# Kernel tuning notes

Measured on AMD Instinct MI355X. Metric: run time of the kernel, lower is better.

## Reference

```python
import jax, jax.numpy as jnp
import numpy as np

B, S, D, H = 16, 512, 1024, 16
DK = D // H
DFF = 4 * D
EPS = 1e-5
NEG = -1e9


def fake_quant(w):
    # EMA int8 symmetric per-tensor fake quantization of weights (inference view)
    scale = jnp.max(jnp.abs(w)) / 127.0
    wq = jnp.round(w / scale) * scale
    # straight-through estimator form (no-op in fwd)
    return w + jax.lax.stop_gradient(wq - w)


def layer_norm(x, g, b):
    mu = jnp.mean(x, axis=-1, keepdims=True)
    var = jnp.mean(jnp.square(x - mu), axis=-1, keepdims=True)
    return (x - mu) * jax.lax.rsqrt(var + EPS) * g + b


def setup_inputs() -> dict:
    key = jax.random.key(0)
    ks = jax.random.split(key, 16)
    std = 0.02
    inp = {
        'x': jax.random.normal(ks[0], (B, S, D), jnp.float32),
        'mask': jax.random.randint(ks[1], (B, 1, S, S), 0, 2, jnp.int32),
        'wq': jax.random.normal(ks[2], (D, D), jnp.float32) * std,
        'bq': jnp.zeros((D,), jnp.float32),
        'wk': jax.random.normal(ks[3], (D, D), jnp.float32) * std,
        'bk': jnp.zeros((D,), jnp.float32),
        'wv': jax.random.normal(ks[4], (D, D), jnp.float32) * std,
        'bv': jnp.zeros((D,), jnp.float32),
        'wo': jax.random.normal(ks[5], (D, D), jnp.float32) * std,
        'bo': jnp.zeros((D,), jnp.float32),
        'w1': jax.random.normal(ks[6], (D, DFF), jnp.float32) * std,
        'b1': jnp.zeros((DFF,), jnp.float32),
        'w2': jax.random.normal(ks[7], (DFF, D), jnp.float32) * std,
        'b2': jnp.zeros((D,), jnp.float32),
        'ln1_g': jnp.ones((D,), jnp.float32),
        'ln1_b': jnp.zeros((D,), jnp.float32),
        'ln2_g': jnp.ones((D,), jnp.float32),
        'ln2_b': jnp.zeros((D,), jnp.float32),
        'layer': 0,
    }
    return inp


def reference(x, mask, wq, bq, wk, bk, wv, bv, wo, bo, w1, b1, w2, b2,
              ln1_g, ln1_b, ln2_g, ln2_b, layer):
    # --- input sublayer: x + attention(LN(x)) (dropout = identity at eval) ---
    h = layer_norm(x, ln1_g, ln1_b)
    q = (h @ fake_quant(wq) + bq).reshape(B, S, H, DK).transpose(0, 2, 1, 3)
    k = (h @ fake_quant(wk) + bk).reshape(B, S, H, DK).transpose(0, 2, 1, 3)
    v = (h @ fake_quant(wv) + bv).reshape(B, S, H, DK).transpose(0, 2, 1, 3)
    scores = jnp.einsum('bhqd,bhkd->bhqk', q, k) * (1.0 / np.sqrt(DK))
    scores = jnp.where(mask == 0, NEG, scores)
    p = jax.nn.softmax(scores, axis=-1)
    attn = jnp.einsum('bhqk,bhkd->bhqd', p, v)
    attn = attn.transpose(0, 2, 1, 3).reshape(B, S, D)
    x = x + (attn @ wo + bo)
    # --- output sublayer: x + FFN(LN(x)), gelu (exact), middle_drop=False ---
    h2 = layer_norm(x, ln2_g, ln2_b)
    ff = jax.nn.gelu(h2 @ w1 + b1, approximate=False) @ w2 + b2
    return x + ff
```

## Files before the change

kernel.cpp:

```cpp
#include <hip/hip_runtime.h>
#include <hip/hip_bf16.h>
#include <math.h>

#define B_   16
#define S_   512
#define D_   1024
#define H_   16
#define DK_  64
#define DFF_ 4096
#define NROW (B_ * S_)
#define NEG_ (-1.0e9f)
#define SCQ_ 0.18033688011112042f

typedef __attribute__((ext_vector_type(8))) short short8v;
typedef __attribute__((ext_vector_type(4))) float f32x4;

__device__ __forceinline__ void load_lds16(const void* g, void* l) {
    __builtin_amdgcn_global_load_lds(
        reinterpret_cast<const __attribute__((address_space(1))) unsigned int*>(
            reinterpret_cast<uintptr_t>(g)),
        reinterpret_cast<__attribute__((address_space(3))) unsigned int*>(
            reinterpret_cast<uintptr_t>(l)),
        16, 0, 0);
}

__device__ __forceinline__ ushort f2bf_raw(float f) {
    __hip_bfloat16 h = __float2bfloat16(f);
    return *(ushort*)&h;
}

__device__ __forceinline__ float gelu_f(float v) {
    return 0.5f * v * (1.0f + erff(v * 0.70710678118654752f));
}

__global__ void zero_scales_k(unsigned int* p) {
    if (threadIdx.x < 3) p[threadIdx.x] = 0u;
}

__global__ void maxabs_k(const float* __restrict__ w, unsigned int* __restrict__ out, int n) {
    float m = 0.f;
    for (int i = blockIdx.x * blockDim.x + threadIdx.x; i < n; i += gridDim.x * blockDim.x)
        m = fmaxf(m, fabsf(w[i]));
#pragma unroll
    for (int off = 1; off < 64; off <<= 1)
        m = fmaxf(m, __shfl_xor(m, off));
    __shared__ float red[4];
    const int wave = threadIdx.x >> 6;
    if ((threadIdx.x & 63) == 0) red[wave] = m;
    __syncthreads();
    if (threadIdx.x == 0) {
        m = fmaxf(fmaxf(red[0], red[1]), fmaxf(red[2], red[3]));
        atomicMax(out, __float_as_uint(m));
    }
}

__global__ __launch_bounds__(256) void maskpack_k(
    const int* __restrict__ mask, unsigned long long* __restrict__ bits) {
    const int g = blockIdx.x * 4 + (threadIdx.x >> 6);
    const unsigned long long bm = __ballot(mask[(size_t)g * 64 + (threadIdx.x & 63)] != 0);
    if ((threadIdx.x & 63) == 0) bits[g] = bm;
}

__global__ __launch_bounds__(256) void transq_k(
    const float* __restrict__ W, const unsigned int* __restrict__ smax,
    __hip_bfloat16* __restrict__ Wt, int K, int N)
{
    __shared__ float t[32][33];
    const int n0 = blockIdx.x * 32, k0 = blockIdx.y * 32;
    const int tx = threadIdx.x, ty = threadIdx.y;
    float scale = 1.0f;
    if (smax) scale = __uint_as_float(*smax) * (1.0f / 127.0f);
#pragma unroll
    for (int i = 0; i < 4; ++i) {
        float v = W[(size_t)(k0 + ty + 8 * i) * N + n0 + tx];
        if (smax) v = rintf(v / scale) * scale;
        t[ty + 8 * i][tx] = v;
    }
    __syncthreads();
#pragma unroll
    for (int i = 0; i < 4; ++i)
        Wt[(size_t)(n0 + ty + 8 * i) * K + k0 + tx] = __float2bfloat16(t[tx][ty + 8 * i]);
}

__global__ __launch_bounds__(256) void ln_bf16_k(
    const float* __restrict__ x, const float* __restrict__ g,
    const float* __restrict__ b, __hip_bfloat16* __restrict__ y)
{
    const int row = blockIdx.x;
    const int tid = threadIdx.x;
    const float4 v = *(const float4*)&x[(size_t)row * D_ + tid * 4];

    float s = v.x + v.y + v.z + v.w;
#pragma unroll
    for (int off = 1; off < 64; off <<= 1) s += __shfl_xor(s, off);
    __shared__ float red[8];
    const int wave = tid >> 6, lane = tid & 63;
    if (lane == 0) red[wave] = s;
    __syncthreads();
    s = red[0] + red[1] + red[2] + red[3];
    const float mu = s * (1.0f / (float)D_);

    const float d0 = v.x - mu, d1 = v.y - mu, d2 = v.z - mu, d3 = v.w - mu;
    float sq = d0 * d0 + d1 * d1 + d2 * d2 + d3 * d3;
#pragma unroll
    for (int off = 1; off < 64; off <<= 1) sq += __shfl_xor(sq, off);
    if (lane == 0) red[4 + wave] = sq;
    __syncthreads();
    sq = red[4] + red[5] + red[6] + red[7];
    const float rs = 1.0f / sqrtf(sq * (1.0f / (float)D_) + 1e-5f);

    const float4 gv = *(const float4*)&g[tid * 4];
    const float4 bv = *(const float4*)&b[tid * 4];
    union { ushort4 u4; ushort u[4]; } cv;
    cv.u[0] = f2bf_raw(d0 * rs * gv.x + bv.x);
    cv.u[1] = f2bf_raw(d1 * rs * gv.y + bv.y);
    cv.u[2] = f2bf_raw(d2 * rs * gv.z + bv.z);
    cv.u[3] = f2bf_raw(d3 * rs * gv.w + bv.w);
    *(ushort4*)&y[(size_t)row * D_ + tid * 4] = cv.u4;
}

template <int BNT, int EPI>
__global__ __launch_bounds__(512, 2) void gemm256(
    const __hip_bfloat16* __restrict__ A, const __hip_bfloat16* __restrict__ Bt,
    const float* __restrict__ bias, const float* __restrict__ bias2,
    const float* __restrict__ bias3, const float* __restrict__ res,
    void* __restrict__ C, void* __restrict__ C2, void* __restrict__ C3,
    int M, int N, int K)
{
    constexpr int BN   = BNT * 64;
    constexpr int ABYT = 256 * 128;
    constexpr int BBYT = BN * 128;
    constexpr int BUF  = ABYT + BBYT;
    constexpr int SB   = BNT / 2;
    __shared__ __align__(16) char smem[2 * BUF];

    const int tid = threadIdx.x;
    const int w = tid >> 6, lane = tid & 63;
    const int llo = lane & 15, lhi = lane >> 4;
    const int wr = w >> 2, wc = w & 3;

    const int nwg = gridDim.x;
    const int bid = blockIdx.x;
    const int swz = (bid & 7) * (nwg >> 3) + (bid >> 3);
    const int nby = M >> 8;
    const int by = swz % nby, bx = swz / nby;
    const int row0 = by * 256, col0 = bx * BN;

    const int cko0 = ((lhi) ^ (llo & 7)) * 16;
    const int cko1 = ((4 + lhi) ^ (llo & 7)) * 16;

    const int l3 = lane >> 3;
    const int klog8 = ((lane & 7) ^ l3) * 8;
    const int rA_base = ((w >> 1) & 3) * 16 + (w & 1) * 8 + l3;
    const int rB_ws = w * 8 + l3;

    const __hip_bfloat16* Asrc[2][2];
#pragma unroll
    for (int h = 0; h < 2; ++h)
#pragma unroll
        for (int s = 0; s < 2; ++s)
            Asrc[h][s] = A + (size_t)(row0 + s * 128 + h * 64 + rA_base) * K + klog8;
    const __hip_bfloat16* Bsrc[2][2];
#pragma unroll
    for (int h = 0; h < 2; ++h)
#pragma unroll
        for (int s = 0; s < 2; ++s)
            Bsrc[h][s] = Bt + (size_t)(col0 + h * (BN / 2) + (SB == 2 ? s * 64 : 0) + rB_ws) * K + klog8;

#define STAGE_A(bufv, hh, tt) do {                                                            \
    load_lds16(Asrc[hh][0] + (size_t)(tt) * 64, smem + (bufv) * BUF + (hh) * 16384 + w * 1024);        \
    load_lds16(Asrc[hh][1] + (size_t)(tt) * 64, smem + (bufv) * BUF + (hh) * 16384 + 8192 + w * 1024); \
} while (0)
#define STAGE_B(bufv, hh, tt) do {                                                                     \
    load_lds16(Bsrc[hh][0] + (size_t)(tt) * 64, smem + (bufv) * BUF + ABYT + (hh) * (BBYT / 2) + w * 1024); \
    if (SB == 2)                                                                                       \
        load_lds16(Bsrc[hh][1] + (size_t)(tt) * 64, smem + (bufv) * BUF + ABYT + (hh) * (BBYT / 2) + 8192 + w * 1024); \
} while (0)

    f32x4 acc[8][BNT] = {};
    const int NT = K >> 6;

    STAGE_B(0, 0, 0); STAGE_B(0, 1, 0); STAGE_A(0, 0, 0); STAGE_A(0, 1, 0);
    asm volatile("s_waitcnt vmcnt(0)");
    __builtin_amdgcn_s_barrier();

    short8v bfr[BNT][2];
    for (int t = 0; t < NT; ++t) {
        const int buf = t & 1;
        const bool more = (t + 1) < NT;
        char* const base = smem + buf * BUF;
#pragma unroll
        for (int ph = 0; ph < 4; ++ph) {
            if (ph == 0) {
#pragma unroll
                for (int n = 0; n < BNT; ++n) {
                    const int brow = wc * (BNT * 16) + n * 16 + llo;
                    bfr[n][0] = *(const short8v*)(base + ABYT + brow * 128 + cko0);
                    bfr[n][1] = *(const short8v*)(base + ABYT + brow * 128 + cko1);
                }
            }
            const int mf0 = ph * 2, mf1 = ph * 2 + 1;
            const int slot0 = (mf0 >> 2) * 128 + wr * 64 + (mf0 & 3) * 16 + llo;
            const int slot1 = (mf1 >> 2) * 128 + wr * 64 + (mf1 & 3) * 16 + llo;
            const short8v a0k0 = *(const short8v*)(base + slot0 * 128 + cko0);
            const short8v a0k1 = *(const short8v*)(base + slot0 * 128 + cko1);
            const short8v a1k0 = *(const short8v*)(base + slot1 * 128 + cko0);
            const short8v a1k1 = *(const short8v*)(base + slot1 * 128 + cko1);
            if (more) {
                if (ph == 0) { STAGE_B(buf ^ 1, 0, t + 1); STAGE_B(buf ^ 1, 1, t + 1); }
                else if (ph == 1) { STAGE_A(buf ^ 1, 0, t + 1); STAGE_A(buf ^ 1, 1, t + 1); }
            }
            __builtin_amdgcn_s_barrier();
            __builtin_amdgcn_s_setprio(1);
#pragma unroll
            for (int n = 0; n < BNT; ++n) {
                acc[mf0][n] = __builtin_amdgcn_mfma_f32_16x16x32_bf16(a0k0, bfr[n][0], acc[mf0][n], 0, 0, 0);
                acc[mf0][n] = __builtin_amdgcn_mfma_f32_16x16x32_bf16(a0k1, bfr[n][1], acc[mf0][n], 0, 0, 0);
                acc[mf1][n] = __builtin_amdgcn_mfma_f32_16x16x32_bf16(a1k0, bfr[n][0], acc[mf1][n], 0, 0, 0);
                acc[mf1][n] = __builtin_amdgcn_mfma_f32_16x16x32_bf16(a1k1, bfr[n][1], acc[mf1][n], 0, 0, 0);
            }
            __builtin_amdgcn_s_setprio(0);
            if (ph == 3) { asm volatile("s_waitcnt vmcnt(0)"); }
            __builtin_amdgcn_s_barrier();
        }
    }
#undef STAGE_A
#undef STAGE_B

    if (EPI == 3) {
#pragma unroll
        for (int n = 0; n < BNT; ++n) {
            const int col = col0 + wc * (BNT * 16) + n * 16 + llo;
            const int proj = col0 >> 10;
            const int lcol = col & 1023;
            const float bs = (proj == 0 ? bias : proj == 1 ? bias2 : bias3)[lcol];
#pragma unroll
            for (int mf = 0; mf < 8; ++mf) {
                const int rbase = row0 + wr * 128 + mf * 16 + lhi * 4;
                if (proj == 2) {
                    const int bb = rbase >> 9, srow = rbase & 511;
                    const int hh = lcol >> 6, dk = lcol & 63;
                    union { ushort4 u4; ushort u[4]; } pk;
#pragma unroll
                    for (int j = 0; j < 4; ++j) pk.u[j] = f2bf_raw(acc[mf][n][j] + bs);
                    *(ushort4*)&((ushort*)C3)[(((size_t)(bb * 16 + hh) * 64 + dk) << 9) + srow] = pk.u4;
                } else {
                    __hip_bfloat16* dst = proj == 0 ? (__hip_bfloat16*)C : (__hip_bfloat16*)C2;
                    const float sc = proj == 0 ? SCQ_ : 1.0f;
#pragma unroll
                    for (int j = 0; j < 4; ++j)
                        dst[(size_t)(rbase + j) * D_ + lcol] = __float2bfloat16((acc[mf][n][j] + bs) * sc);
                }
            }
        }
    } else {
        constexpr int WCOL = BNT * 16;
        constexpr int ESTR = WCOL + 4;
        float* const eslab = (float*)smem + w * (16 * ESTR);
        const int rr = lane >> 2;
        const int cq = lane & 3;
        const int c0 = cq * (BNT * 4);
        const int gcolb = col0 + wc * WCOL + c0;
#pragma unroll
        for (int mf = 0; mf < 8; ++mf) {
#pragma unroll
            for (int n = 0; n < BNT; ++n)
#pragma unroll
                for (int j = 0; j < 4; ++j)
                    eslab[(lhi * 4 + j) * ESTR + n * 16 + llo] = acc[mf][n][j];
            const int grow = row0 + wr * 128 + mf * 16 + rr;
            if (EPI == 1) {
                ushort tmp[BNT * 4];
#pragma unroll
                for (int i = 0; i < BNT; ++i) {
                    float4 v = *(float4*)&eslab[rr * ESTR + c0 + i * 4];
                    const float4 b4 = *(const float4*)&bias[gcolb + i * 4];
                    tmp[i * 4 + 0] = f2bf_raw(gelu_f(v.x + b4.x));
                    tmp[i * 4 + 1] = f2bf_raw(gelu_f(v.y + b4.y));
                    tmp[i * 4 + 2] = f2bf_raw(gelu_f(v.z + b4.z));
                    tmp[i * 4 + 3] = f2bf_raw(gelu_f(v.w + b4.w));
                }
                ushort* dst = (ushort*)C + (size_t)grow * N + gcolb;
#pragma unroll
                for (int i = 0; i < BNT / 2; ++i)
                    *(short8v*)(dst + i * 8) = *(short8v*)&tmp[i * 8];
            } else {
#pragma unroll
                for (int i = 0; i < BNT; ++i) {
                    float4 v = *(float4*)&eslab[rr * ESTR + c0 + i * 4];
                    const float4 b4 = *(const float4*)&bias[gcolb + i * 4];
                    const float4 r4 = *(const float4*)&res[(size_t)grow * N + gcolb + i * 4];
                    v.x += b4.x + r4.x;
                    v.y += b4.y + r4.y;
                    v.z += b4.z + r4.z;
                    v.w += b4.w + r4.w;
                    *(float4*)&((float*)C)[(size_t)grow * N + gcolb + i * 4] = v;
                }
            }
        }
    }
}

__global__ __launch_bounds__(256) void attn_mfma_k(
    const __hip_bfloat16* __restrict__ q, const __hip_bfloat16* __restrict__ k,
    const __hip_bfloat16* __restrict__ vt, const unsigned long long* __restrict__ mbits,
    __hip_bfloat16* __restrict__ o)
{
    const int qt = blockIdx.x;
    const int bh = blockIdx.y;
    const int b = bh >> 4, h = bh & 15;

    __shared__ __align__(16) __hip_bfloat16 Qs[64 * 72];
    __shared__ __align__(16) __hip_bfloat16 Ks[64 * 72];
    __shared__ __align__(16) __hip_bfloat16 Vts[64 * 72];
    __shared__ __align__(16) __hip_bfloat16 Pt[64 * 72];

    const int tid = threadIdx.x;
    const int w = tid >> 6, l = tid & 63;
    const int llo = l & 15, lhi = l >> 4;
    const int srow = tid >> 2, schk = tid & 3;

    {
        const __hip_bfloat16* qg =
            q + (size_t)(b * S_ + qt * 64 + srow) * D_ + h * 64 + schk * 16;
        *(short8v*)&Qs[srow * 72 + schk * 16] = *(const short8v*)qg;
        *(short8v*)&Qs[srow * 72 + schk * 16 + 8] = *(const short8v*)(qg + 8);
    }

    const __hip_bfloat16* kptr = k + (size_t)(b * S_ + srow) * D_ + h * 64 + schk * 16;
    const __hip_bfloat16* vptr = vt + (((size_t)(b * 16 + h) * 64 + srow) << 9) + schk * 16;
    short8v kr0 = *(const short8v*)kptr;
    short8v kr1 = *(const short8v*)(kptr + 8);
    short8v vr0 = *(const short8v*)vptr;
    short8v vr1 = *(const short8v*)(vptr + 8);

    __syncthreads();

    const short8v qa0 = *(const short8v*)&Qs[(w * 16 + llo) * 72 + lhi * 8];
    const short8v qa1 = *(const short8v*)&Qs[(w * 16 + llo) * 72 + 32 + lhi * 8];

    const unsigned long long* mrow =
        mbits + (((size_t)(b * S_ + qt * 64 + w * 16 + lhi * 4)) << 3);

    f32x4 oacc[4] = {};
    float m_r[4] = {-INFINITY, -INFINITY, -INFINITY, -INFINITY};
    float l_r[4] = {0.f, 0.f, 0.f, 0.f};

    for (int kt = 0; kt < 8; ++kt) {
        *(short8v*)&Ks[srow * 72 + schk * 16] = kr0;
        *(short8v*)&Ks[srow * 72 + schk * 16 + 8] = kr1;
        *(short8v*)&Vts[srow * 72 + schk * 16] = vr0;
        *(short8v*)&Vts[srow * 72 + schk * 16 + 8] = vr1;
        __syncthreads();

        short8v nk0, nk1, nv0, nv1;
        if (kt < 7) {
            const __hip_bfloat16* kp = kptr + (size_t)(kt + 1) * (64 * D_);
            const __hip_bfloat16* vp = vptr + (kt + 1) * 64;
            nk0 = *(const short8v*)kp;
            nk1 = *(const short8v*)(kp + 8);
            nv0 = *(const short8v*)vp;
            nv1 = *(const short8v*)(vp + 8);
        }

        f32x4 sacc[4] = {};
#pragma unroll
        for (int n = 0; n < 4; ++n)
            sacc[n] = __builtin_amdgcn_mfma_f32_16x16x32_bf16(
                qa0, *(const short8v*)&Ks[(n * 16 + llo) * 72 + lhi * 8], sacc[n], 0, 0, 0);
#pragma unroll
        for (int n = 0; n < 4; ++n)
            sacc[n] = __builtin_amdgcn_mfma_f32_16x16x32_bf16(
                qa1, *(const short8v*)&Ks[(n * 16 + llo) * 72 + 32 + lhi * 8], sacc[n], 0, 0, 0);

#pragma unroll
        for (int j = 0; j < 4; ++j) {
            const unsigned long long mb = mrow[j * 8 + kt];
            const float s0 = ((mb >> llo) & 1ull)        ? sacc[0][j] : NEG_;
            const float s1 = ((mb >> (llo + 16)) & 1ull) ? sacc[1][j] : NEG_;
            const float s2 = ((mb >> (llo + 32)) & 1ull) ? sacc[2][j] : NEG_;
            const float s3 = ((mb >> (llo + 48)) & 1ull) ? sacc[3][j] : NEG_;
            float pm = fmaxf(fmaxf(s0, s1), fmaxf(s2, s3));
            pm = fmaxf(pm, __shfl_xor(pm, 1));
            pm = fmaxf(pm, __shfl_xor(pm, 2));
            pm = fmaxf(pm, __shfl_xor(pm, 4));
            pm = fmaxf(pm, __shfl_xor(pm, 8));
            const float mnew = fmaxf(m_r[j], pm);
            const float alpha = exp2f(m_r[j] - mnew);
            const float p0 = exp2f(s0 - mnew);
            const float p1 = exp2f(s1 - mnew);
            const float p2 = exp2f(s2 - mnew);
            const float p3 = exp2f(s3 - mnew);
            float rsum = p0 + p1 + p2 + p3;
            rsum += __shfl_xor(rsum, 1);
            rsum += __shfl_xor(rsum, 2);
            rsum += __shfl_xor(rsum, 4);
            rsum += __shfl_xor(rsum, 8);
            l_r[j] = l_r[j] * alpha + rsum;
            m_r[j] = mnew;
#pragma unroll
            for (int df = 0; df < 4; ++df) oacc[df][j] *= alpha;
            const int prow = (w * 16 + lhi * 4 + j) * 72;
            Pt[prow + llo]      = __float2bfloat16(p0);
            Pt[prow + llo + 16] = __float2bfloat16(p1);
            Pt[prow + llo + 32] = __float2bfloat16(p2);
            Pt[prow + llo + 48] = __float2bfloat16(p3);
        }

#pragma unroll
        for (int ks = 0; ks < 2; ++ks) {
            const short8v pa = *(const short8v*)&Pt[(w * 16 + llo) * 72 + ks * 32 + lhi * 8];
#pragma unroll
            for (int df = 0; df < 4; ++df) {
                const short8v vb = *(const short8v*)&Vts[(df * 16 + llo) * 72 + ks * 32 + lhi * 8];
                oacc[df] = __builtin_amdgcn_mfma_f32_16x16x32_bf16(pa, vb, oacc[df], 0, 0, 0);
            }
        }
        __syncthreads();

        if (kt < 7) { kr0 = nk0; kr1 = nk1; vr0 = nv0; vr1 = nv1; }
    }

#pragma unroll
    for (int j = 0; j < 4; ++j) {
        const float inv = 1.0f / l_r[j];
        __hip_bfloat16* orow =
            o + (size_t)(b * S_ + qt * 64 + w * 16 + lhi * 4 + j) * D_ + h * 64;
#pragma unroll
        for (int df = 0; df < 4; ++df)
            orow[df * 16 + llo] = __float2bfloat16(oacc[df][j] * inv);
    }
}

extern "C" void kernel_launch(void* const* d_in, const int* in_sizes, int n_in,
                              void* d_out, int out_size, void* d_ws, size_t ws_size,
                              hipStream_t stream)
{
    const float* x    = (const float*)d_in[0];
    const int*   mask = (const int*)d_in[1];
    const float* wq   = (const float*)d_in[2];
    const float* bq   = (const float*)d_in[3];
    const float* wk   = (const float*)d_in[4];
    const float* bk   = (const float*)d_in[5];
    const float* wv   = (const float*)d_in[6];
    const float* bv   = (const float*)d_in[7];
    const float* wo   = (const float*)d_in[8];
    const float* bo   = (const float*)d_in[9];
    const float* w1   = (const float*)d_in[10];
    const float* b1   = (const float*)d_in[11];
    const float* w2   = (const float*)d_in[12];
    const float* b2   = (const float*)d_in[13];
    const float* ln1g = (const float*)d_in[14];
    const float* ln1b = (const float*)d_in[15];
    const float* ln2g = (const float*)d_in[16];
    const float* ln2b = (const float*)d_in[17];
    float* out = (float*)d_out;
    char* ws = (char*)d_ws;

    const size_t MB = 1024 * 1024;
    __hip_bfloat16* hb    = (__hip_bfloat16*)(ws);
    __hip_bfloat16* qbh   = (__hip_bfloat16*)(ws + 16 * MB);
    __hip_bfloat16* kbh   = (__hip_bfloat16*)(ws + 32 * MB);
    __hip_bfloat16* vth   = (__hip_bfloat16*)(ws + 48 * MB);
    __hip_bfloat16* attnb = (__hip_bfloat16*)(ws + 64 * MB);
    __hip_bfloat16* ff1b  = (__hip_bfloat16*)(ws + 16 * MB);
    __hip_bfloat16* wcat  = (__hip_bfloat16*)(ws + 80 * MB);
    __hip_bfloat16* fqqt  = (__hip_bfloat16*)(ws + 80 * MB);
    __hip_bfloat16* fqkt  = (__hip_bfloat16*)(ws + 82 * MB);
    __hip_bfloat16* fqvt  = (__hip_bfloat16*)(ws + 84 * MB);
    __hip_bfloat16* wot   = (__hip_bfloat16*)(ws + 86 * MB);
    __hip_bfloat16* w1t   = (__hip_bfloat16*)(ws + 88 * MB);
    __hip_bfloat16* w2t   = (__hip_bfloat16*)(ws + 96 * MB);
    unsigned int*   scales = (unsigned int*)(ws + 104 * MB);
    unsigned long long* mbits = (unsigned long long*)(ws + 105 * MB);

    const int NW = D_ * D_;

    zero_scales_k<<<1, 64, 0, stream>>>(scales);
    maxabs_k<<<256, 256, 0, stream>>>(wq, scales + 0, NW);
    maxabs_k<<<256, 256, 0, stream>>>(wk, scales + 1, NW);
    maxabs_k<<<256, 256, 0, stream>>>(wv, scales + 2, NW);
    maskpack_k<<<(B_ * S_ * (S_ / 64)) / 4, 256, 0, stream>>>(mask, mbits);

    const dim3 tb(32, 8);
    transq_k<<<dim3(D_ / 32, D_ / 32), tb, 0, stream>>>(wq, scales + 0, fqqt, D_, D_);
    transq_k<<<dim3(D_ / 32, D_ / 32), tb, 0, stream>>>(wk, scales + 1, fqkt, D_, D_);
    transq_k<<<dim3(D_ / 32, D_ / 32), tb, 0, stream>>>(wv, scales + 2, fqvt, D_, D_);
    transq_k<<<dim3(D_ / 32, D_ / 32), tb, 0, stream>>>(wo, nullptr, wot, D_, D_);
    transq_k<<<dim3(DFF_ / 32, D_ / 32), tb, 0, stream>>>(w1, nullptr, w1t, D_, DFF_);
    transq_k<<<dim3(D_ / 32, DFF_ / 32), tb, 0, stream>>>(w2, nullptr, w2t, DFF_, D_);

    ln_bf16_k<<<NROW, 256, 0, stream>>>(x, ln1g, ln1b, hb);

    gemm256<4, 3><<<(3 * D_ / 256) * (NROW / 256), 512, 0, stream>>>(
        hb, wcat, bq, bk, bv, nullptr, qbh, kbh, vth, NROW, 3 * D_, D_);

    attn_mfma_k<<<dim3(S_ / 64, B_ * H_), 256, 0, stream>>>(qbh, kbh, vth, mbits, attnb);

    gemm256<2, 2><<<(D_ / 128) * (NROW / 256), 512, 0, stream>>>(
        attnb, wot, bo, nullptr, nullptr, x, out, nullptr, nullptr, NROW, D_, D_);

    ln_bf16_k<<<NROW, 256, 0, stream>>>(out, ln2g, ln2b, hb);

    gemm256<4, 1><<<(DFF_ / 256) * (NROW / 256), 512, 0, stream>>>(
        hb, w1t, b1, nullptr, nullptr, nullptr, ff1b, nullptr, nullptr, NROW, DFF_, D_);

    gemm256<2, 2><<<(D_ / 128) * (NROW / 256), 512, 0, stream>>>(
        ff1b, w2t, b2, nullptr, nullptr, out, out, nullptr, nullptr, NROW, D_, DFF_);
}
```

Baseline: 452.9 us.

## Merge weight-prep kernels into fewer launches and skip redundant softmax rescales

```diff
diff --git a/kernel.cpp b/kernel.cpp
--- a/kernel.cpp
+++ b/kernel.cpp
@@ -33,11 +33,20 @@
     return 0.5f * v * (1.0f + erff(v * 0.70710678118654752f));
 }
 
-__global__ void zero_scales_k(unsigned int* p) {
-    if (threadIdx.x < 3) p[threadIdx.x] = 0u;
-}
-
-__global__ void maxabs_k(const float* __restrict__ w, unsigned int* __restrict__ out, int n) {
+__global__ __launch_bounds__(256) void maskpack_k(
+    const int* __restrict__ mask, unsigned long long* __restrict__ bits,
+    unsigned int* __restrict__ scales) {
+    if (blockIdx.x == 0 && threadIdx.x < 3) scales[threadIdx.x] = 0u;
+    const int g = blockIdx.x * 4 + (threadIdx.x >> 6);
+    const unsigned long long bm = __ballot(mask[(size_t)g * 64 + (threadIdx.x & 63)] != 0);
+    if ((threadIdx.x & 63) == 0) bits[g] = bm;
+}
+
+__global__ __launch_bounds__(256) void maxabs3_k(
+    const float* __restrict__ wq, const float* __restrict__ wk,
+    const float* __restrict__ wv, unsigned int* __restrict__ out, int n) {
+    const int wi = blockIdx.y;
+    const float* w = wi == 0 ? wq : (wi == 1 ? wk : wv);
     float m = 0.f;
     for (int i = blockIdx.x * blockDim.x + threadIdx.x; i < n; i += gridDim.x * blockDim.x)
         m = fmaxf(m, fabsf(w[i]));
@@ -50,30 +59,38 @@
     __syncthreads();
     if (threadIdx.x == 0) {
         m = fmaxf(fmaxf(red[0], red[1]), fmaxf(red[2], red[3]));
-        atomicMax(out, __float_as_uint(m));
-    }
-}
-
-__global__ __launch_bounds__(256) void maskpack_k(
-    const int* __restrict__ mask, unsigned long long* __restrict__ bits) {
-    const int g = blockIdx.x * 4 + (threadIdx.x >> 6);
-    const unsigned long long bm = __ballot(mask[(size_t)g * 64 + (threadIdx.x & 63)] != 0);
-    if ((threadIdx.x & 63) == 0) bits[g] = bm;
-}
-
-__global__ __launch_bounds__(256) void transq_k(
-    const float* __restrict__ W, const unsigned int* __restrict__ smax,
-    __hip_bfloat16* __restrict__ Wt, int K, int N)
+        atomicMax(out + wi, __float_as_uint(m));
+    }
+}
+
+__global__ __launch_bounds__(256) void transq_all_k(
+    const float* __restrict__ wq, const float* __restrict__ wk,
+    const float* __restrict__ wv, const float* __restrict__ wo,
+    const float* __restrict__ w1, const float* __restrict__ w2,
+    const unsigned int* __restrict__ scales,
+    __hip_bfloat16* __restrict__ wcat,
+    __hip_bfloat16* __restrict__ wot,
+    __hip_bfloat16* __restrict__ w1t, __hip_bfloat16* __restrict__ w2t)
 {
+    const int bid = blockIdx.x;
+    int wi, rem, nbn, K, N;
+    if (bid < 4096)      { wi = bid >> 10; rem = bid & 1023; nbn = 32;  K = 1024; N = 1024; }
+    else if (bid < 8192) { wi = 4; rem = bid - 4096;         nbn = 128; K = 1024; N = 4096; }
+    else                 { wi = 5; rem = bid - 8192;         nbn = 32;  K = 4096; N = 1024; }
+    const float* W = wi == 0 ? wq : wi == 1 ? wk : wi == 2 ? wv : wi == 3 ? wo : wi == 4 ? w1 : w2;
+    __hip_bfloat16* Wt = wi < 3 ? wcat + (size_t)wi * 1024 * 1024
+                       : wi == 3 ? wot : wi == 4 ? w1t : w2t;
+    const int n0 = (rem % nbn) * 32, k0 = (rem / nbn) * 32;
+
     __shared__ float t[32][33];
-    const int n0 = blockIdx.x * 32, k0 = blockIdx.y * 32;
     const int tx = threadIdx.x, ty = threadIdx.y;
     float scale = 1.0f;
-    if (smax) scale = __uint_as_float(*smax) * (1.0f / 127.0f);
+    const bool doq = wi < 3;
+    if (doq) scale = __uint_as_float(scales[wi]) * (1.0f / 127.0f);
 #pragma unroll
     for (int i = 0; i < 4; ++i) {
         float v = W[(size_t)(k0 + ty + 8 * i) * N + n0 + tx];
-        if (smax) v = rintf(v / scale) * scale;
+        if (doq) v = rintf(v / scale) * scale;
         t[ty + 8 * i][tx] = v;
     }
     __syncthreads();
@@ -385,21 +402,24 @@
             pm = fmaxf(pm, __shfl_xor(pm, 2));
             pm = fmaxf(pm, __shfl_xor(pm, 4));
             pm = fmaxf(pm, __shfl_xor(pm, 8));
-            const float mnew = fmaxf(m_r[j], pm);
-            const float alpha = exp2f(m_r[j] - mnew);
-            const float p0 = exp2f(s0 - mnew);
-            const float p1 = exp2f(s1 - mnew);
-            const float p2 = exp2f(s2 - mnew);
-            const float p3 = exp2f(s3 - mnew);
+            float alpha = 1.0f;
+            if (!__all(pm <= m_r[j] + 8.0f)) {
+                const float mnew = fmaxf(m_r[j], pm);
+                alpha = exp2f(m_r[j] - mnew);
+                m_r[j] = mnew;
+#pragma unroll
+                for (int df = 0; df < 4; ++df) oacc[df][j] *= alpha;
+            }
+            const float p0 = exp2f(s0 - m_r[j]);
+            const float p1 = exp2f(s1 - m_r[j]);
+            const float p2 = exp2f(s2 - m_r[j]);
+            const float p3 = exp2f(s3 - m_r[j]);
             float rsum = p0 + p1 + p2 + p3;
             rsum += __shfl_xor(rsum, 1);
             rsum += __shfl_xor(rsum, 2);
             rsum += __shfl_xor(rsum, 4);
             rsum += __shfl_xor(rsum, 8);
             l_r[j] = l_r[j] * alpha + rsum;
-            m_r[j] = mnew;
-#pragma unroll
-            for (int df = 0; df < 4; ++df) oacc[df][j] *= alpha;
             const int prow = (w * 16 + lhi * 4 + j) * 72;
             Pt[prow + llo]      = __float2bfloat16(p0);
             Pt[prow + llo + 16] = __float2bfloat16(p1);
@@ -465,30 +485,16 @@
     __hip_bfloat16* attnb = (__hip_bfloat16*)(ws + 64 * MB);
     __hip_bfloat16* ff1b  = (__hip_bfloat16*)(ws + 16 * MB);
     __hip_bfloat16* wcat  = (__hip_bfloat16*)(ws + 80 * MB);
-    __hip_bfloat16* fqqt  = (__hip_bfloat16*)(ws + 80 * MB);
-    __hip_bfloat16* fqkt  = (__hip_bfloat16*)(ws + 82 * MB);
-    __hip_bfloat16* fqvt  = (__hip_bfloat16*)(ws + 84 * MB);
     __hip_bfloat16* wot   = (__hip_bfloat16*)(ws + 86 * MB);
     __hip_bfloat16* w1t   = (__hip_bfloat16*)(ws + 88 * MB);
     __hip_bfloat16* w2t   = (__hip_bfloat16*)(ws + 96 * MB);
     unsigned int*   scales = (unsigned int*)(ws + 104 * MB);
     unsigned long long* mbits = (unsigned long long*)(ws + 105 * MB);
 
-    const int NW = D_ * D_;
-
-    zero_scales_k<<<1, 64, 0, stream>>>(scales);
-    maxabs_k<<<256, 256, 0, stream>>>(wq, scales + 0, NW);
-    maxabs_k<<<256, 256, 0, stream>>>(wk, scales + 1, NW);
-    maxabs_k<<<256, 256, 0, stream>>>(wv, scales + 2, NW);
-    maskpack_k<<<(B_ * S_ * (S_ / 64)) / 4, 256, 0, stream>>>(mask, mbits);
-
-    const dim3 tb(32, 8);
-    transq_k<<<dim3(D_ / 32, D_ / 32), tb, 0, stream>>>(wq, scales + 0, fqqt, D_, D_);
-    transq_k<<<dim3(D_ / 32, D_ / 32), tb, 0, stream>>>(wk, scales + 1, fqkt, D_, D_);
-    transq_k<<<dim3(D_ / 32, D_ / 32), tb, 0, stream>>>(wv, scales + 2, fqvt, D_, D_);
-    transq_k<<<dim3(D_ / 32, D_ / 32), tb, 0, stream>>>(wo, nullptr, wot, D_, D_);
-    transq_k<<<dim3(DFF_ / 32, D_ / 32), tb, 0, stream>>>(w1, nullptr, w1t, D_, DFF_);
-    transq_k<<<dim3(D_ / 32, DFF_ / 32), tb, 0, stream>>>(w2, nullptr, w2t, DFF_, D_);
+    maskpack_k<<<(B_ * S_ * (S_ / 64)) / 4, 256, 0, stream>>>(mask, mbits, scales);
+    maxabs3_k<<<dim3(256, 3), 256, 0, stream>>>(wq, wk, wv, scales, D_ * D_);
+    transq_all_k<<<12288, dim3(32, 8), 0, stream>>>(
+        wq, wk, wv, wo, w1, w2, scales, wcat, wot, w1t, w2t);
 
     ln_bf16_k<<<NROW, 256, 0, stream>>>(x, ln1g, ln1b, hb);
 
```

Result: faster. 420.3 us, median of 2 (-7.2%).
